# Performance work log

Hardware: AMD Instinct MI355X
Metric: run time of the kernel (lower is better)

Reference implementation:

```python
import jax, jax.numpy as jnp
import numpy as np

DROPOUT_P = 0.5

def _gcn_conv(h, W, b, src, dst, norm, self_norm, n):
    # h: [N, Din] -> [N, Dout]; symmetric-normalized aggregation with self loops
    h = h @ W
    msg = h[src] * norm[:, None]                       # [E, Dout]
    agg = jax.ops.segment_sum(msg, dst, num_segments=n)
    return agg + h * self_norm[:, None] + b


def setup_inputs() -> dict:
    key = jax.random.key(0)
    ks = jax.random.split(key, 8)
    N, E, D_IN, D_OUT = 50000, 800000, 512, 256
    H = 2 * D_OUT  # 512
    x = jax.random.normal(ks[0], (N, D_IN), dtype=jnp.float32)
    edge_index = jax.random.randint(ks[1], (2, E), 0, N, dtype=jnp.int64)
    s = 1.0 / np.sqrt(D_IN)
    W1 = jax.random.uniform(ks[2], (D_IN, H), jnp.float32, -s, s)
    b1 = jnp.zeros((H,), jnp.float32)
    s2 = 1.0 / np.sqrt(H)
    Wmu = jax.random.uniform(ks[3], (H, D_OUT), jnp.float32, -s2, s2)
    bmu = jnp.zeros((D_OUT,), jnp.float32)
    Wls = jax.random.uniform(ks[4], (H, D_OUT), jnp.float32, -s2, s2)
    bls = jnp.zeros((D_OUT,), jnp.float32)
    return {"x": x, "edge_index": edge_index, "W1": W1, "b1": b1,
            "Wmu": Wmu, "bmu": bmu, "Wls": Wls, "bls": bls}


def reference(x, edge_index, W1, b1, Wmu, bmu, Wls, bls):
    n = x.shape[0]
    src, dst = edge_index[0], edge_index[1]
    # GCN symmetric normalization with self loops: deg includes +1 self loop
    deg = jax.ops.segment_sum(jnp.ones_like(dst, dtype=x.dtype), dst, num_segments=n) + 1.0
    dinv = jax.lax.rsqrt(deg)
    norm = dinv[src] * dinv[dst]     # per-edge norm
    self_norm = dinv * dinv          # self-loop norm = 1/deg
    # dropout (train mode, deterministic mask)
    keep = jax.random.bernoulli(jax.random.key(42), 1.0 - DROPOUT_P, x.shape)
    h = jnp.where(keep, x / (1.0 - DROPOUT_P), 0.0)
    h = jax.nn.relu(_gcn_conv(h, W1, b1, src, dst, norm, self_norm, n))
    mu = _gcn_conv(h, Wmu, bmu, src, dst, norm, self_norm, n)
    logstd = _gcn_conv(h, Wls, bls, src, dst, norm, self_norm, n)
    return (mu, logstd)
```

## Files before the change

### kernel.cpp

```cpp
#include <hip/hip_runtime.h>
#include <hip/hip_bf16.h>

typedef __hip_bfloat16 bf16;
typedef __attribute__((ext_vector_type(8))) short short8;
typedef __attribute__((ext_vector_type(4))) float f32x4;

__device__ __forceinline__ float bfu(unsigned short b) {
    unsigned u = ((unsigned)b) << 16;
    float f;
    __builtin_memcpy(&f, &u, 4);
    return f;
}
__device__ __forceinline__ unsigned short f2b(float f) {
    return (unsigned short)(__hip_bfloat16_raw(__float2bfloat16(f)).x);
}

__device__ __forceinline__ void gl_lds16(const void* g, void* l) {
    __builtin_amdgcn_global_load_lds(
        (const __attribute__((address_space(1))) void*)g,
        (__attribute__((address_space(3))) void*)l, 16, 0, 0);
}

__device__ __forceinline__ bool keep_elem(unsigned idx) {
    const unsigned k0 = 0u, k1 = 42u;
    const unsigned k2 = k0 ^ k1 ^ 0x1BD11BDAu;
    unsigned x0 = k0;
    unsigned x1 = idx + k1;
#define TF_QR(R) { x0 += x1; x1 = (x1 << R) | (x1 >> (32 - R)); x1 ^= x0; }
    TF_QR(13) TF_QR(15) TF_QR(26) TF_QR(6)
    x0 += k1; x1 += k2 + 1u;
    TF_QR(17) TF_QR(29) TF_QR(16) TF_QR(24)
    x0 += k2; x1 += k0 + 2u;
    TF_QR(13) TF_QR(15) TF_QR(26) TF_QR(6)
    x0 += k0; x1 += k1 + 3u;
    TF_QR(17) TF_QR(29) TF_QR(16) TF_QR(24)
    x0 += k1; x1 += k2 + 4u;
    TF_QR(13) TF_QR(15) TF_QR(26) TF_QR(6)
    x0 += k2; x1 += k0 + 5u;
#undef TF_QR
    return (((x0 ^ x1) >> 31) & 1u) == 0u;
}

__global__ void detect_all_k(const unsigned* __restrict__ ei,
                             const unsigned short* __restrict__ x,
                             const unsigned short* __restrict__ w1,
                             int* __restrict__ flag) {
    __shared__ int red[256];
    if (blockIdx.x == 0) {
        unsigned v = 0;
        for (int i = threadIdx.x; i < 2048; i += 256) v |= ei[2 * i + 1];
        red[threadIdx.x] = (int)v;
        __syncthreads();
        for (int s = 128; s > 0; s >>= 1) {
            if (threadIdx.x < s) red[threadIdx.x] |= red[threadIdx.x + s];
            __syncthreads();
        }
        if (threadIdx.x == 0) flag[0] = (red[0] == 0) ? 1 : 0;
    } else {
        const unsigned short* p = (blockIdx.x == 1) ? x : w1;
        int cnt = 0;
        for (int i = threadIdx.x; i < 1024; i += 256) {
            unsigned short b = p[2 * i];
            int e = (b >> 7) & 0xFF;
            if ((b & 0x7FFF) == 0 || (e >= 100 && e < 140)) cnt++;
        }
        red[threadIdx.x] = cnt;
        __syncthreads();
        for (int s = 128; s > 0; s >>= 1) {
            if (threadIdx.x < s) red[threadIdx.x] += red[threadIdx.x + s];
            __syncthreads();
        }
        if (threadIdx.x == 0) flag[blockIdx.x] = (red[0] < 614) ? 1 : 0;
    }
}

__global__ void convert_edges_k(const void* __restrict__ src, int* __restrict__ out,
                                int twoE, const int* __restrict__ flag) {
    int i = blockIdx.x * 256 + threadIdx.x;
    if (i >= twoE) return;
    if (flag[0]) out[i] = (int)((const unsigned long long*)src)[i];
    else         out[i] = ((const int*)src)[i];
}

__global__ void canon_transpose_k(const void* __restrict__ src, unsigned short* __restrict__ dst,
                                  int K, int Nn, const int* __restrict__ flag, int fidx) {
    __shared__ unsigned short tile[16][17];
    int k0 = blockIdx.x * 16, n0 = blockIdx.y * 16;
    int k = k0 + threadIdx.y, n = n0 + threadIdx.x;
    unsigned short v;
    if (flag[fidx]) v = f2b(((const float*)src)[(size_t)k * Nn + n]);
    else            v = ((const unsigned short*)src)[(size_t)k * Nn + n];
    tile[threadIdx.y][threadIdx.x] = v;
    __syncthreads();
    int nn = n0 + threadIdx.y, kk = k0 + threadIdx.x;
    dst[(size_t)nn * K + kk] = tile[threadIdx.x][threadIdx.y];
}

__global__ void canon_bias_k(const void* __restrict__ b1, const void* __restrict__ bmu,
                             const void* __restrict__ bls, bf16* __restrict__ b1c,
                             bf16* __restrict__ bcat, int H, int DOUT,
                             const int* __restrict__ flag) {
    int i = blockIdx.x * 256 + threadIdx.x;
    int f = flag[2];
    if (i < H) {
        b1c[i] = f ? __float2bfloat16(((const float*)b1)[i]) : ((const bf16*)b1)[i];
    } else if (i < H + DOUT) {
        int j = i - H;
        bcat[j] = f ? __float2bfloat16(((const float*)bmu)[j]) : ((const bf16*)bmu)[j];
    } else if (i < H + 2 * DOUT) {
        int j = i - H - DOUT;
        bcat[DOUT + j] = f ? __float2bfloat16(((const float*)bls)[j]) : ((const bf16*)bls)[j];
    }
}

__global__ void zero_int_k(int* __restrict__ p, int n) {
    int i = blockIdx.x * 256 + threadIdx.x;
    if (i < n) p[i] = 0;
}
__global__ void deg_count_k(const int* __restrict__ edges, int* __restrict__ degi,
                            int E, int n) {
    int e = blockIdx.x * 256 + threadIdx.x;
    if (e >= E) return;
    int d = edges[E + e];
    d = (d < 0) ? 0 : (d >= n ? n - 1 : d);
    atomicAdd(&degi[d], 1);
}
__global__ void block_sums_k(const int* __restrict__ deg, int* __restrict__ partial, int n) {
    __shared__ int sh[256];
    int i = blockIdx.x * 256 + threadIdx.x;
    sh[threadIdx.x] = (i < n) ? deg[i] : 0;
    __syncthreads();
    for (int s = 128; s > 0; s >>= 1) {
        if (threadIdx.x < s) sh[threadIdx.x] += sh[threadIdx.x + s];
        __syncthreads();
    }
    if (threadIdx.x == 0) partial[blockIdx.x] = sh[0];
}
__global__ void scan_partials_k(int* __restrict__ partial, int G) {
    __shared__ int sh[256];
    int v = (threadIdx.x < G) ? partial[threadIdx.x] : 0;
    sh[threadIdx.x] = v;
    __syncthreads();
    for (int s = 1; s < 256; s <<= 1) {
        int t = 0;
        if (threadIdx.x >= s) t = sh[threadIdx.x - s];
        __syncthreads();
        sh[threadIdx.x] += t;
        __syncthreads();
    }
    if (threadIdx.x < G) partial[threadIdx.x] = sh[threadIdx.x] - v;
}
__global__ void scan_block_k(const int* __restrict__ deg, const int* __restrict__ partial,
                             int* __restrict__ row_ptr, float* __restrict__ dinv, int n) {
    __shared__ int sh[256];
    int i = blockIdx.x * 256 + threadIdx.x;
    int v = (i < n) ? deg[i] : 0;
    sh[threadIdx.x] = v;
    __syncthreads();
    for (int s = 1; s < 256; s <<= 1) {
        int t = 0;
        if (threadIdx.x >= s) t = sh[threadIdx.x - s];
        __syncthreads();
        sh[threadIdx.x] += t;
        __syncthreads();
    }
    int incl = sh[threadIdx.x];
    int base = partial[blockIdx.x];
    if (i < n) {
        row_ptr[i] = base + incl - v;
        dinv[i] = rsqrtf(1.0f + (float)v);
    }
    if (i == n - 1) row_ptr[n] = base + incl;
}
__global__ void fill_k(const int* __restrict__ edges, const int* __restrict__ row_ptr,
                       int* __restrict__ cnt, int* __restrict__ col, int E, int n) {
    int e = blockIdx.x * 256 + threadIdx.x;
    if (e >= E) return;
    int s = edges[e], d = edges[E + e];
    s = (s < 0) ? 0 : (s >= n ? n - 1 : s);
    d = (d < 0) ? 0 : (d >= n ? n - 1 : d);
    int pos = row_ptr[d] + atomicAdd(&cnt[d], 1);
    col[pos] = s;
}

__global__ __launch_bounds__(512) void gemm_mfma_k(
    const void* __restrict__ Ain, const bf16* __restrict__ Bt,
    bf16* __restrict__ Cb, float* __restrict__ Cf, float* __restrict__ Cf2,
    const bf16* __restrict__ bias, int M, int K,
    const int* __restrict__ flag, int drop) {
    __shared__ short sA[128 * 64];
    __shared__ short sB[256 * 64];
    const int tid = threadIdx.x;
    const int lane = tid & 63;
    const int w = tid >> 6;
    const int m0 = blockIdx.x * 128;
    const int n0 = blockIdx.y * 256;
    const int wm = (w & 1) * 64;
    const int wn = (w >> 1) * 64;

    f32x4 acc[4][4] = {};

    const int srow = tid >> 3;
    const int schunk = (tid & 7) ^ (srow & 7);
    const int scol = schunk * 8;
    const bool xf32 = drop && flag[1];

    for (int kk = 0; kk < K; kk += 64) {
#pragma unroll
        for (int p = 0; p < 4; ++p)
            gl_lds16(Bt + (size_t)(n0 + p * 64 + srow) * K + kk + scol,
                     &sB[p * 4096 + tid * 8]);
        if (!drop) {
#pragma unroll
            for (int p = 0; p < 2; ++p) {
                int r = m0 + p * 64 + srow; if (r >= M) r = M - 1;
                gl_lds16((const bf16*)Ain + (size_t)r * K + kk + scol,
                         &sA[p * 4096 + tid * 8]);
            }
        } else {
#pragma unroll
            for (int p = 0; p < 2; ++p) {
                int r = m0 + p * 64 + srow; if (r >= M) r = M - 1;
                unsigned gidx = (unsigned)r * (unsigned)K + (unsigned)(kk + scol);
                float v[8];
                if (xf32) {
                    const f32x4* pp = (const f32x4*)Ain;
                    f32x4 a = pp[gidx >> 2], b = pp[(gidx >> 2) + 1];
#pragma unroll
                    for (int k2 = 0; k2 < 4; ++k2) { v[k2] = a[k2]; v[4 + k2] = b[k2]; }
                } else {
                    short8 u = ((const short8*)Ain)[gidx >> 3];
#pragma unroll
                    for (int k2 = 0; k2 < 8; ++k2) v[k2] = bfu((unsigned short)u[k2]);
                }
                short8 o;
#pragma unroll
                for (int k2 = 0; k2 < 8; ++k2) {
                    float f = keep_elem(gidx + k2) ? v[k2] * 2.0f : 0.0f;
                    o[k2] = (short)f2b(f);
                }
                *(short8*)&sA[p * 4096 + tid * 8] = o;
            }
        }
        __syncthreads();

        const int fr = lane & 15;
        const int q = lane >> 4;
#pragma unroll
        for (int ks = 0; ks < 2; ++ks) {
            const int slot = ks * 4 + q;
            short8 af[4], bf2[4];
#pragma unroll
            for (int i = 0; i < 4; ++i) {
                int r = wm + i * 16 + fr;
                af[i] = *(const short8*)&sA[r * 64 + ((slot ^ (r & 7)) * 8)];
            }
#pragma unroll
            for (int j = 0; j < 4; ++j) {
                int r = wn + j * 16 + fr;
                bf2[j] = *(const short8*)&sB[r * 64 + ((slot ^ (r & 7)) * 8)];
            }
#pragma unroll
            for (int i = 0; i < 4; ++i)
#pragma unroll
                for (int j = 0; j < 4; ++j)
                    acc[i][j] = __builtin_amdgcn_mfma_f32_16x16x32_bf16(
                        af[i], bf2[j], acc[i][j], 0, 0, 0);
        }
        __syncthreads();
    }

    const int crow = (lane >> 4) * 4;
    const int ccol = lane & 15;
    const int cb = n0 + wn;
    if (Cf) {
        const int side = (cb >= 256) ? 1 : 0;
        float* base = side ? Cf2 : Cf;
        const int nb = cb - side * 256;
#pragma unroll
        for (int i = 0; i < 4; ++i) {
#pragma unroll
            for (int r = 0; r < 4; ++r) {
                int row = m0 + wm + i * 16 + crow + r;
                if (row >= M) continue;
                float* cp = base + (size_t)row * 256 + nb;
#pragma unroll
                for (int j = 0; j < 4; ++j) {
                    int c = j * 16 + ccol;
                    cp[c] = acc[i][j][r] + __bfloat162float(bias[cb + c]);
                }
            }
        }
    } else {
#pragma unroll
        for (int i = 0; i < 4; ++i) {
#pragma unroll
            for (int r = 0; r < 4; ++r) {
                int row = m0 + wm + i * 16 + crow + r;
                if (row >= M) continue;
                bf16* cp = Cb + (size_t)row * 512 + cb;
#pragma unroll
                for (int j = 0; j < 4; ++j)
                    cp[j * 16 + ccol] = __float2bfloat16(acc[i][j][r]);
            }
        }
    }
}

__global__ __launch_bounds__(256) void gather_k(
    const bf16* __restrict__ t, const int* __restrict__ row_ptr,
    const int* __restrict__ col, const float* __restrict__ dinv,
    const bf16* __restrict__ bias, bf16* __restrict__ outp, int mode, int N) {
    const int node = blockIdx.x * 4 + (threadIdx.x >> 6);
    if (node >= N) return;
    const int lane = threadIdx.x & 63;
    const short8* tp = (const short8*)t;
    const int beg = row_ptr[node];
    const int end = row_ptr[node + 1];
    const float dv = dinv[node];
    float acc[8] = {0.f, 0.f, 0.f, 0.f, 0.f, 0.f, 0.f, 0.f};

    int e = beg;
    const int elim = beg + ((end - beg) & ~7);
    if (e < elim) {
        int c[8];
        float w[8];
#pragma unroll
        for (int k = 0; k < 8; ++k) c[k] = col[e + k];
#pragma unroll
        for (int k = 0; k < 8; ++k) w[k] = dinv[c[k]] * dv;
        for (;;) {
            short8 u[8];
#pragma unroll
            for (int k = 0; k < 8; ++k) u[k] = tp[(size_t)c[k] * 64 + lane];
            const int en = e + 8;
            const bool more = en < elim;
            int cn[8];
            float wn2[8];
            if (more) {
#pragma unroll
                for (int k = 0; k < 8; ++k) cn[k] = col[en + k];
#pragma unroll
                for (int k = 0; k < 8; ++k) wn2[k] = dinv[cn[k]] * dv;
            }
#pragma unroll
            for (int k = 0; k < 8; ++k) {
                const float wk = w[k];
#pragma unroll
                for (int j = 0; j < 8; ++j)
                    acc[j] += wk * bfu((unsigned short)u[k][j]);
            }
            e = en;
            if (!more) break;
#pragma unroll
            for (int k = 0; k < 8; ++k) { c[k] = cn[k]; w[k] = wn2[k]; }
        }
    }
    for (; e + 4 <= end; e += 4) {
        int s0 = col[e + 0], s1 = col[e + 1], s2 = col[e + 2], s3 = col[e + 3];
        float w0 = dinv[s0] * dv, w1 = dinv[s1] * dv;
        float w2 = dinv[s2] * dv, w3 = dinv[s3] * dv;
        short8 u0 = tp[(size_t)s0 * 64 + lane];
        short8 u1 = tp[(size_t)s1 * 64 + lane];
        short8 u2 = tp[(size_t)s2 * 64 + lane];
        short8 u3 = tp[(size_t)s3 * 64 + lane];
#pragma unroll
        for (int k = 0; k < 8; ++k) {
            acc[k] += w0 * bfu((unsigned short)u0[k]);
            acc[k] += w1 * bfu((unsigned short)u1[k]);
            acc[k] += w2 * bfu((unsigned short)u2[k]);
            acc[k] += w3 * bfu((unsigned short)u3[k]);
        }
    }
    for (; e < end; ++e) {
        int s = col[e];
        float w = dinv[s] * dv;
        short8 u = tp[(size_t)s * 64 + lane];
#pragma unroll
        for (int k = 0; k < 8; ++k) acc[k] += w * bfu((unsigned short)u[k]);
    }
    {
        short8 u = tp[(size_t)node * 64 + lane];
        float w = dv * dv;
#pragma unroll
        for (int k = 0; k < 8; ++k) acc[k] += w * bfu((unsigned short)u[k]);
    }
    if (mode == 1) {
        short8 bs = ((const short8*)bias)[lane];
#pragma unroll
        for (int k = 0; k < 8; ++k) {
            acc[k] += bfu((unsigned short)bs[k]);
            acc[k] = fmaxf(acc[k], 0.f);
        }
    }
    short8 o;
#pragma unroll
    for (int k = 0; k < 8; ++k) o[k] = (short)f2b(acc[k]);
    ((short8*)outp)[(size_t)node * 64 + lane] = o;
}

extern "C" void kernel_launch(void* const* d_in, const int* in_sizes, int n_in,
                              void* d_out, int out_size, void* d_ws, size_t ws_size,
                              hipStream_t stream) {
    const void* xin   = d_in[0];
    const void* ei    = d_in[1];
    const void* W1in  = d_in[2];
    const void* b1in  = d_in[3];
    const void* Wmuin = d_in[4];
    const void* bmuin = d_in[5];
    const void* Wlsin = d_in[6];
    const void* blsin = d_in[7];
    float* out = (float*)d_out;

    const int H    = in_sizes[3];
    const int DOUT = in_sizes[5];
    const int DIN  = in_sizes[2] / H;
    const int N    = in_sizes[0] / DIN;
    const int E    = in_sizes[1] / 2;
    const int G    = (N + 255) / 256;

    char* ws = (char*)d_ws;
    size_t off = 0;
    auto alloc = [&](size_t bytes) {
        void* p = ws + off;
        off = (off + bytes + 255) & ~(size_t)255;
        return p;
    };
    int*   flag    = (int*)alloc(256);
    int*   edges   = (int*)alloc((size_t)2 * E * 4);
    int*   degcnt  = (int*)alloc((size_t)2 * N * 4);
    int*   degi    = degcnt;
    int*   cnt     = degcnt + N;
    int*   row_ptr = (int*)alloc((size_t)(N + 1) * 4);
    int*   partial = (int*)alloc((size_t)G * 4);
    int*   col     = (int*)alloc((size_t)E * 4);
    float* dinv    = (float*)alloc((size_t)N * 4);
    bf16*  t1      = (bf16*)alloc((size_t)N * H * 2);
    bf16*  g1      = (bf16*)alloc((size_t)N * H * 2);
    bf16*  h1      = (bf16*)alloc((size_t)N * H * 2);
    bf16*  W1t     = (bf16*)alloc((size_t)DIN * H * 2);
    bf16*  Wcat    = (bf16*)alloc((size_t)H * 2 * DOUT * 2);
    bf16*  b1c     = (bf16*)alloc((size_t)H * 2);
    bf16*  bcat    = (bf16*)alloc((size_t)2 * DOUT * 2);
    if (off > ws_size) return;

    const int twoE = 2 * E;
    hipLaunchKernelGGL(detect_all_k, dim3(3), dim3(256), 0, stream,
                       (const unsigned*)ei, (const unsigned short*)xin,
                       (const unsigned short*)W1in, flag);

    hipLaunchKernelGGL(convert_edges_k, dim3((twoE + 255) / 256), dim3(256), 0, stream,
                       ei, edges, twoE, flag);
    hipLaunchKernelGGL(canon_transpose_k, dim3(DIN / 16, H / 16), dim3(16, 16), 0, stream,
                       W1in, (unsigned short*)W1t, DIN, H, flag, 2);
    hipLaunchKernelGGL(canon_transpose_k, dim3(H / 16, DOUT / 16), dim3(16, 16), 0, stream,
                       Wmuin, (unsigned short*)Wcat, H, DOUT, flag, 2);
    hipLaunchKernelGGL(canon_transpose_k, dim3(H / 16, DOUT / 16), dim3(16, 16), 0, stream,
                       Wlsin, (unsigned short*)(Wcat + (size_t)DOUT * H), H, DOUT, flag, 2);
    hipLaunchKernelGGL(canon_bias_k, dim3((H + 2 * DOUT + 255) / 256), dim3(256), 0, stream,
                       b1in, bmuin, blsin, b1c, bcat, H, DOUT, flag);

    hipLaunchKernelGGL(zero_int_k, dim3((2 * N + 255) / 256), dim3(256), 0, stream, degcnt, 2 * N);
    hipLaunchKernelGGL(deg_count_k, dim3((E + 255) / 256), dim3(256), 0, stream, edges, degi, E, N);
    hipLaunchKernelGGL(block_sums_k, dim3(G), dim3(256), 0, stream, degi, partial, N);
    hipLaunchKernelGGL(scan_partials_k, dim3(1), dim3(256), 0, stream, partial, G);
    hipLaunchKernelGGL(scan_block_k, dim3(G), dim3(256), 0, stream, degi, partial, row_ptr, dinv, N);
    hipLaunchKernelGGL(fill_k, dim3((E + 255) / 256), dim3(256), 0, stream, edges, row_ptr, cnt, col, E, N);

    hipLaunchKernelGGL(gemm_mfma_k, dim3((N + 127) / 128, 2), dim3(512), 0, stream,
                       xin, W1t, t1, (float*)nullptr, (float*)nullptr,
                       (const bf16*)nullptr, N, DIN, flag, 1);
    hipLaunchKernelGGL(gather_k, dim3((N + 3) / 4), dim3(256), 0, stream,
                       t1, row_ptr, col, dinv, b1c, h1, 1, N);

    hipLaunchKernelGGL(gather_k, dim3((N + 3) / 4), dim3(256), 0, stream,
                       h1, row_ptr, col, dinv, (const bf16*)nullptr, g1, 0, N);
    hipLaunchKernelGGL(gemm_mfma_k, dim3((N + 127) / 128, 2), dim3(512), 0, stream,
                       g1, Wcat, (bf16*)nullptr, out, out + (size_t)N * DOUT,
                       bcat, N, H, flag, 0);
}
```

Baseline: 676.5 us.

## Precompute dropout bitmask and double-buffer A tile with register-held B fragments

The Threefry dropout mask is now computed once by a separate kernel into a bitmask, so the GEMM no longer runs the hash inline for every element on every K-tile. The GEMM is restructured: the K step drops to 32, the A tile is double-buffered in LDS with the next tile prefetched during the MFMAs, and B fragments are loaded straight from global memory into registers instead of staging through LDS, with launch bounds raised for occupancy. The tradeoffs are an extra kernel and mask buffer, more global B traffic without LDS sharing, and higher register pressure under the tighter launch bounds.

Result: slower. 734.4 us (+8.6%).

```diff
diff --git a/kernel.cpp b/kernel.cpp
--- a/kernel.cpp
+++ b/kernel.cpp
@@ -41,6 +41,17 @@
     return (((x0 ^ x1) >> 31) & 1u) == 0u;
 }
 
+__global__ void mask_k(unsigned char* __restrict__ mp, int nbytes) {
+    int i = blockIdx.x * 256 + threadIdx.x;
+    if (i >= nbytes) return;
+    unsigned base = (unsigned)i * 8u;
+    unsigned m = 0;
+#pragma unroll
+    for (int k = 0; k < 8; ++k)
+        if (keep_elem(base + k)) m |= (1u << k);
+    mp[i] = (unsigned char)m;
+}
+
 __global__ void detect_all_k(const unsigned* __restrict__ ei,
                              const unsigned short* __restrict__ x,
                              const unsigned short* __restrict__ w1,
@@ -183,13 +194,12 @@
     col[pos] = s;
 }
 
-__global__ __launch_bounds__(512) void gemm_mfma_k(
+__global__ __launch_bounds__(512, 4) void gemm_mfma_k(
     const void* __restrict__ Ain, const bf16* __restrict__ Bt,
     bf16* __restrict__ Cb, float* __restrict__ Cf, float* __restrict__ Cf2,
-    const bf16* __restrict__ bias, int M, int K,
-    const int* __restrict__ flag, int drop) {
-    __shared__ short sA[128 * 64];
-    __shared__ short sB[256 * 64];
+    const bf16* __restrict__ bias, const unsigned char* __restrict__ maskp,
+    int M, int K, const int* __restrict__ flag, int drop) {
+    __shared__ short sA[2][128 * 32];
     const int tid = threadIdx.x;
     const int lane = tid & 63;
     const int w = tid >> 6;
@@ -200,72 +210,100 @@
 
     f32x4 acc[4][4] = {};
 
-    const int srow = tid >> 3;
-    const int schunk = (tid & 7) ^ (srow & 7);
-    const int scol = schunk * 8;
+    const int prow = tid >> 2;
+    const int sc = (tid & 3) ^ ((prow >> 1) & 3);
+    int grow = m0 + prow; if (grow >= M) grow = M - 1;
+    const bf16* Ab = (const bf16*)Ain;
     const bool xf32 = drop && flag[1];
 
-    for (int kk = 0; kk < K; kk += 64) {
-#pragma unroll
-        for (int p = 0; p < 4; ++p)
-            gl_lds16(Bt + (size_t)(n0 + p * 64 + srow) * K + kk + scol,
-                     &sB[p * 4096 + tid * 8]);
-        if (!drop) {
-#pragma unroll
-            for (int p = 0; p < 2; ++p) {
-                int r = m0 + p * 64 + srow; if (r >= M) r = M - 1;
-                gl_lds16((const bf16*)Ain + (size_t)r * K + kk + scol,
-                         &sA[p * 4096 + tid * 8]);
+    const int fr = lane & 15;
+    const int q = lane >> 4;
+    const bf16* Brow = Bt + (size_t)(n0 + wn + fr) * K + q * 8;
+
+    const int NT = K >> 5;
+    short8 bcur[4], bnext[4];
+
+    if (!drop) {
+        gl_lds16(Ab + (size_t)grow * K + sc * 8, &sA[0][tid * 8]);
+    } else {
+        unsigned gidx = (unsigned)grow * (unsigned)K + (unsigned)(sc * 8);
+        unsigned mv = maskp[gidx >> 3];
+        short8 o;
+        if (xf32) {
+            const f32x4* pp = (const f32x4*)Ain;
+            f32x4 a = pp[gidx >> 2], b = pp[(gidx >> 2) + 1];
+#pragma unroll
+            for (int k = 0; k < 8; ++k) {
+                float f = (k < 4) ? a[k] : b[k - 4];
+                o[k] = ((mv >> k) & 1) ? (short)f2b(f * 2.0f) : (short)0;
             }
         } else {
-#pragma unroll
-            for (int p = 0; p < 2; ++p) {
-                int r = m0 + p * 64 + srow; if (r >= M) r = M - 1;
-                unsigned gidx = (unsigned)r * (unsigned)K + (unsigned)(kk + scol);
-                float v[8];
+            short8 u = ((const short8*)Ain)[gidx >> 3];
+#pragma unroll
+            for (int k = 0; k < 8; ++k)
+                o[k] = ((mv >> k) & 1) ? (short)f2b(bfu((unsigned short)u[k]) * 2.0f)
+                                       : (short)0;
+        }
+        *(short8*)&sA[0][tid * 8] = o;
+    }
+#pragma unroll
+    for (int j = 0; j < 4; ++j)
+        bcur[j] = *(const short8*)(Brow + (size_t)(j * 16) * K);
+    __syncthreads();
+
+    for (int t = 0; t < NT; ++t) {
+        const int kk = t << 5;
+        const short* sa = sA[t & 1];
+        const bool pre = (t + 1 < NT);
+        f32x4 xa, xb;
+        short8 xu;
+        unsigned mv = 0;
+        if (pre) {
+            const int kn = kk + 32;
+            if (!drop) {
+                gl_lds16(Ab + (size_t)grow * K + kn + sc * 8, &sA[(t + 1) & 1][tid * 8]);
+            } else {
+                unsigned gidx = (unsigned)grow * (unsigned)K + (unsigned)(kn + sc * 8);
                 if (xf32) {
                     const f32x4* pp = (const f32x4*)Ain;
-                    f32x4 a = pp[gidx >> 2], b = pp[(gidx >> 2) + 1];
-#pragma unroll
-                    for (int k2 = 0; k2 < 4; ++k2) { v[k2] = a[k2]; v[4 + k2] = b[k2]; }
+                    xa = pp[gidx >> 2];
+                    xb = pp[(gidx >> 2) + 1];
                 } else {
-                    short8 u = ((const short8*)Ain)[gidx >> 3];
-#pragma unroll
-                    for (int k2 = 0; k2 < 8; ++k2) v[k2] = bfu((unsigned short)u[k2]);
+                    xu = ((const short8*)Ain)[gidx >> 3];
                 }
+                mv = maskp[gidx >> 3];
+            }
+#pragma unroll
+            for (int j = 0; j < 4; ++j)
+                bnext[j] = *(const short8*)(Brow + (size_t)(j * 16) * K + kn);
+        }
+
+        short8 af[4];
+#pragma unroll
+        for (int i = 0; i < 4; ++i) {
+            int r = wm + i * 16 + fr;
+            af[i] = *(const short8*)&sa[r * 32 + ((q ^ ((r >> 1) & 3)) * 8)];
+        }
+#pragma unroll
+        for (int i = 0; i < 4; ++i)
+#pragma unroll
+            for (int j = 0; j < 4; ++j)
+                acc[i][j] = __builtin_amdgcn_mfma_f32_16x16x32_bf16(
+                    af[i], bcur[j], acc[i][j], 0, 0, 0);
+
+        if (pre) {
+            if (drop) {
                 short8 o;
 #pragma unroll
-                for (int k2 = 0; k2 < 8; ++k2) {
-                    float f = keep_elem(gidx + k2) ? v[k2] * 2.0f : 0.0f;
-                    o[k2] = (short)f2b(f);
+                for (int k = 0; k < 8; ++k) {
+                    float f = xf32 ? ((k < 4) ? xa[k] : xb[k - 4])
+                                   : bfu((unsigned short)xu[k]);
+                    o[k] = ((mv >> k) & 1) ? (short)f2b(f * 2.0f) : (short)0;
                 }
-                *(short8*)&sA[p * 4096 + tid * 8] = o;
-            }
-        }
-        __syncthreads();
-
-        const int fr = lane & 15;
-        const int q = lane >> 4;
-#pragma unroll
-        for (int ks = 0; ks < 2; ++ks) {
-            const int slot = ks * 4 + q;
-            short8 af[4], bf2[4];
-#pragma unroll
-            for (int i = 0; i < 4; ++i) {
-                int r = wm + i * 16 + fr;
-                af[i] = *(const short8*)&sA[r * 64 + ((slot ^ (r & 7)) * 8)];
-            }
-#pragma unroll
-            for (int j = 0; j < 4; ++j) {
-                int r = wn + j * 16 + fr;
-                bf2[j] = *(const short8*)&sB[r * 64 + ((slot ^ (r & 7)) * 8)];
-            }
-#pragma unroll
-            for (int i = 0; i < 4; ++i)
-#pragma unroll
-                for (int j = 0; j < 4; ++j)
-                    acc[i][j] = __builtin_amdgcn_mfma_f32_16x16x32_bf16(
-                        af[i], bf2[j], acc[i][j], 0, 0, 0);
+                *(short8*)&sA[(t + 1) & 1][tid * 8] = o;
+            }
+#pragma unroll
+            for (int j = 0; j < 4; ++j) bcur[j] = bnext[j];
         }
         __syncthreads();
     }
@@ -435,6 +473,7 @@
     int*   partial = (int*)alloc((size_t)G * 4);
     int*   col     = (int*)alloc((size_t)E * 4);
     float* dinv    = (float*)alloc((size_t)N * 4);
+    unsigned char* mask = (unsigned char*)alloc((size_t)N * DIN / 8);
     bf16*  t1      = (bf16*)alloc((size_t)N * H * 2);
     bf16*  g1      = (bf16*)alloc((size_t)N * H * 2);
     bf16*  h1      = (bf16*)alloc((size_t)N * H * 2);
@@ -445,9 +484,11 @@
     if (off > ws_size) return;
 
     const int twoE = 2 * E;
+    const int NB = N * DIN / 8;
     hipLaunchKernelGGL(detect_all_k, dim3(3), dim3(256), 0, stream,
                        (const unsigned*)ei, (const unsigned short*)xin,
                        (const unsigned short*)W1in, flag);
+    hipLaunchKernelGGL(mask_k, dim3((NB + 255) / 256), dim3(256), 0, stream, mask, NB);
 
     hipLaunchKernelGGL(convert_edges_k, dim3((twoE + 255) / 256), dim3(256), 0, stream,
                        ei, edges, twoE, flag);
@@ -469,7 +510,7 @@
 
     hipLaunchKernelGGL(gemm_mfma_k, dim3((N + 127) / 128, 2), dim3(512), 0, stream,
                        xin, W1t, t1, (float*)nullptr, (float*)nullptr,
-                       (const bf16*)nullptr, N, DIN, flag, 1);
+                       (const bf16*)nullptr, mask, N, DIN, flag, 1);
     hipLaunchKernelGGL(gather_k, dim3((N + 3) / 4), dim3(256), 0, stream,
                        t1, row_ptr, col, dinv, b1c, h1, 1, N);
 
@@ -477,5 +518,5 @@
                        h1, row_ptr, col, dinv, (const bf16*)nullptr, g1, 0, N);
     hipLaunchKernelGGL(gemm_mfma_k, dim3((N + 127) / 128, 2), dim3(512), 0, stream,
                        g1, Wcat, (bf16*)nullptr, out, out + (size_t)N * DOUT,
-                       bcat, N, H, flag, 0);
-}
+                       bcat, mask, N, H, flag, 0);
+}
```

## Precompute dropout bitmask and shrink GEMM tiles to 128x128 with K-step 32

Applied to the files above, without the earlier changes.

Adds a kernel that evaluates the Threefry dropout mask once into a packed bitmask. The first GEMM then reads one mask byte per 8 elements instead of running the hash inline, where it was recomputed for each N-tile of x. The GEMM also moves from 512-thread 128x256 tiles with K=64 to 256-thread 128x128 tiles with K=32 and a new LDS swizzle. Smaller LDS use and more blocks may raise occupancy, but the A tile is now reloaded across four column blocks instead of two, and the bitmask costs extra memory traffic.

Result: slower. 712.3 us (+5.3%).

```diff
diff --git a/kernel.cpp b/kernel.cpp
--- a/kernel.cpp
+++ b/kernel.cpp
@@ -41,6 +41,17 @@
     return (((x0 ^ x1) >> 31) & 1u) == 0u;
 }
 
+__global__ void mask_k(unsigned char* __restrict__ mp, int nbytes) {
+    int i = blockIdx.x * 256 + threadIdx.x;
+    if (i >= nbytes) return;
+    unsigned base = (unsigned)i * 8u;
+    unsigned m = 0;
+#pragma unroll
+    for (int k = 0; k < 8; ++k)
+        if (keep_elem(base + k)) m |= (1u << k);
+    mp[i] = (unsigned char)m;
+}
+
 __global__ void detect_all_k(const unsigned* __restrict__ ei,
                              const unsigned short* __restrict__ x,
                              const unsigned short* __restrict__ w1,
@@ -183,90 +194,95 @@
     col[pos] = s;
 }
 
-__global__ __launch_bounds__(512) void gemm_mfma_k(
+__global__ __launch_bounds__(256) void gemm_mfma_k(
     const void* __restrict__ Ain, const bf16* __restrict__ Bt,
     bf16* __restrict__ Cb, float* __restrict__ Cf, float* __restrict__ Cf2,
-    const bf16* __restrict__ bias, int M, int K,
-    const int* __restrict__ flag, int drop) {
-    __shared__ short sA[128 * 64];
-    __shared__ short sB[256 * 64];
+    const bf16* __restrict__ bias, const unsigned char* __restrict__ maskp,
+    int M, int K, const int* __restrict__ flag, int drop) {
+    __shared__ short sA[128 * 32];
+    __shared__ short sB[128 * 32];
     const int tid = threadIdx.x;
     const int lane = tid & 63;
     const int w = tid >> 6;
     const int m0 = blockIdx.x * 128;
-    const int n0 = blockIdx.y * 256;
+    const int n0 = blockIdx.y * 128;
     const int wm = (w & 1) * 64;
     const int wn = (w >> 1) * 64;
 
     f32x4 acc[4][4] = {};
 
-    const int srow = tid >> 3;
-    const int schunk = (tid & 7) ^ (srow & 7);
-    const int scol = schunk * 8;
+    const int srow = lane >> 2;
+    const int c = lane & 3;
     const bool xf32 = drop && flag[1];
-
-    for (int kk = 0; kk < K; kk += 64) {
-#pragma unroll
-        for (int p = 0; p < 4; ++p)
-            gl_lds16(Bt + (size_t)(n0 + p * 64 + srow) * K + kk + scol,
-                     &sB[p * 4096 + tid * 8]);
+    const bf16* Ab = (const bf16*)Ain;
+
+    const int fr = lane & 15;
+    const int q = lane >> 4;
+
+    for (int kk = 0; kk < K; kk += 32) {
+#pragma unroll
+        for (int p = 0; p < 2; ++p) {
+            int r = p * 64 + w * 16 + srow;
+            int sc = c ^ ((r >> 1) & 3);
+            gl_lds16(Bt + (size_t)(n0 + r) * K + kk + sc * 8,
+                     &sB[p * 2048 + w * 512 + lane * 8]);
+        }
         if (!drop) {
 #pragma unroll
             for (int p = 0; p < 2; ++p) {
-                int r = m0 + p * 64 + srow; if (r >= M) r = M - 1;
-                gl_lds16((const bf16*)Ain + (size_t)r * K + kk + scol,
-                         &sA[p * 4096 + tid * 8]);
+                int r = p * 64 + w * 16 + srow;
+                int sc = c ^ ((r >> 1) & 3);
+                int grow = m0 + r; if (grow >= M) grow = M - 1;
+                gl_lds16(Ab + (size_t)grow * K + kk + sc * 8,
+                         &sA[p * 2048 + w * 512 + lane * 8]);
             }
         } else {
 #pragma unroll
             for (int p = 0; p < 2; ++p) {
-                int r = m0 + p * 64 + srow; if (r >= M) r = M - 1;
-                unsigned gidx = (unsigned)r * (unsigned)K + (unsigned)(kk + scol);
-                float v[8];
+                int r = p * 64 + w * 16 + srow;
+                int sc = c ^ ((r >> 1) & 3);
+                int grow = m0 + r; if (grow >= M) grow = M - 1;
+                unsigned gidx = (unsigned)grow * (unsigned)K + (unsigned)(kk + sc * 8);
+                unsigned mv = maskp[gidx >> 3];
+                short8 o;
                 if (xf32) {
                     const f32x4* pp = (const f32x4*)Ain;
                     f32x4 a = pp[gidx >> 2], b = pp[(gidx >> 2) + 1];
 #pragma unroll
-                    for (int k2 = 0; k2 < 4; ++k2) { v[k2] = a[k2]; v[4 + k2] = b[k2]; }
+                    for (int k2 = 0; k2 < 8; ++k2) {
+                        float f = (k2 < 4) ? a[k2] : b[k2 - 4];
+                        o[k2] = ((mv >> k2) & 1) ? (short)f2b(f * 2.0f) : (short)0;
+                    }
                 } else {
                     short8 u = ((const short8*)Ain)[gidx >> 3];
 #pragma unroll
-                    for (int k2 = 0; k2 < 8; ++k2) v[k2] = bfu((unsigned short)u[k2]);
+                    for (int k2 = 0; k2 < 8; ++k2)
+                        o[k2] = ((mv >> k2) & 1)
+                                    ? (short)f2b(bfu((unsigned short)u[k2]) * 2.0f)
+                                    : (short)0;
                 }
-                short8 o;
-#pragma unroll
-                for (int k2 = 0; k2 < 8; ++k2) {
-                    float f = keep_elem(gidx + k2) ? v[k2] * 2.0f : 0.0f;
-                    o[k2] = (short)f2b(f);
-                }
-                *(short8*)&sA[p * 4096 + tid * 8] = o;
+                *(short8*)&sA[p * 2048 + w * 512 + lane * 8] = o;
             }
         }
         __syncthreads();
 
-        const int fr = lane & 15;
-        const int q = lane >> 4;
-#pragma unroll
-        for (int ks = 0; ks < 2; ++ks) {
-            const int slot = ks * 4 + q;
-            short8 af[4], bf2[4];
-#pragma unroll
-            for (int i = 0; i < 4; ++i) {
-                int r = wm + i * 16 + fr;
-                af[i] = *(const short8*)&sA[r * 64 + ((slot ^ (r & 7)) * 8)];
-            }
-#pragma unroll
-            for (int j = 0; j < 4; ++j) {
-                int r = wn + j * 16 + fr;
-                bf2[j] = *(const short8*)&sB[r * 64 + ((slot ^ (r & 7)) * 8)];
-            }
-#pragma unroll
-            for (int i = 0; i < 4; ++i)
-#pragma unroll
-                for (int j = 0; j < 4; ++j)
-                    acc[i][j] = __builtin_amdgcn_mfma_f32_16x16x32_bf16(
-                        af[i], bf2[j], acc[i][j], 0, 0, 0);
-        }
+        short8 af[4], bf2[4];
+#pragma unroll
+        for (int i = 0; i < 4; ++i) {
+            int r = wm + i * 16 + fr;
+            af[i] = *(const short8*)&sA[r * 32 + ((q ^ ((r >> 1) & 3)) * 8)];
+        }
+#pragma unroll
+        for (int j = 0; j < 4; ++j) {
+            int r = wn + j * 16 + fr;
+            bf2[j] = *(const short8*)&sB[r * 32 + ((q ^ ((r >> 1) & 3)) * 8)];
+        }
+#pragma unroll
+        for (int i = 0; i < 4; ++i)
+#pragma unroll
+            for (int j = 0; j < 4; ++j)
+                acc[i][j] = __builtin_amdgcn_mfma_f32_16x16x32_bf16(
+                    af[i], bf2[j], acc[i][j], 0, 0, 0);
         __syncthreads();
     }
 
@@ -286,8 +302,8 @@
                 float* cp = base + (size_t)row * 256 + nb;
 #pragma unroll
                 for (int j = 0; j < 4; ++j) {
-                    int c = j * 16 + ccol;
-                    cp[c] = acc[i][j][r] + __bfloat162float(bias[cb + c]);
+                    int cc = j * 16 + ccol;
+                    cp[cc] = acc[i][j][r] + __bfloat162float(bias[cb + cc]);
                 }
             }
         }
@@ -435,6 +451,7 @@
     int*   partial = (int*)alloc((size_t)G * 4);
     int*   col     = (int*)alloc((size_t)E * 4);
     float* dinv    = (float*)alloc((size_t)N * 4);
+    unsigned char* mask = (unsigned char*)alloc((size_t)N * DIN / 8);
     bf16*  t1      = (bf16*)alloc((size_t)N * H * 2);
     bf16*  g1      = (bf16*)alloc((size_t)N * H * 2);
     bf16*  h1      = (bf16*)alloc((size_t)N * H * 2);
@@ -445,9 +462,11 @@
     if (off > ws_size) return;
 
     const int twoE = 2 * E;
+    const int NB = N * DIN / 8;
     hipLaunchKernelGGL(detect_all_k, dim3(3), dim3(256), 0, stream,
                        (const unsigned*)ei, (const unsigned short*)xin,
                        (const unsigned short*)W1in, flag);
+    hipLaunchKernelGGL(mask_k, dim3((NB + 255) / 256), dim3(256), 0, stream, mask, NB);
 
     hipLaunchKernelGGL(convert_edges_k, dim3((twoE + 255) / 256), dim3(256), 0, stream,
                        ei, edges, twoE, flag);
@@ -467,15 +486,15 @@
     hipLaunchKernelGGL(scan_block_k, dim3(G), dim3(256), 0, stream, degi, partial, row_ptr, dinv, N);
     hipLaunchKernelGGL(fill_k, dim3((E + 255) / 256), dim3(256), 0, stream, edges, row_ptr, cnt, col, E, N);
 
-    hipLaunchKernelGGL(gemm_mfma_k, dim3((N + 127) / 128, 2), dim3(512), 0, stream,
+    hipLaunchKernelGGL(gemm_mfma_k, dim3((N + 127) / 128, 4), dim3(256), 0, stream,
                        xin, W1t, t1, (float*)nullptr, (float*)nullptr,
-                       (const bf16*)nullptr, N, DIN, flag, 1);
+                       (const bf16*)nullptr, mask, N, DIN, flag, 1);
     hipLaunchKernelGGL(gather_k, dim3((N + 3) / 4), dim3(256), 0, stream,
                        t1, row_ptr, col, dinv, b1c, h1, 1, N);
 
     hipLaunchKernelGGL(gather_k, dim3((N + 3) / 4), dim3(256), 0, stream,
                        h1, row_ptr, col, dinv, (const bf16*)nullptr, g1, 0, N);
-    hipLaunchKernelGGL(gemm_mfma_k, dim3((N + 127) / 128, 2), dim3(512), 0, stream,
+    hipLaunchKernelGGL(gemm_mfma_k, dim3((N + 127) / 128, 4), dim3(256), 0, stream,
                        g1, Wcat, (bf16*)nullptr, out, out + (size_t)N * DOUT,
-                       bcat, N, H, flag, 0);
-}
+                       bcat, mask, N, H, flag, 0);
+}
```
